# Kernel optimization log

Hardware: AMD Instinct MI355X
Metric: run time of the kernel (lower is better)

Reference implementation:

```python
import jax, jax.numpy as jnp
import numpy as np

N_NODES = 100000
N_EDGES = 262144
IN_DIM = 768
HIDDEN = 256


def setup_inputs() -> dict:
    key = jax.random.key(0)
    ks = jax.random.split(key, 8)
    x_src = jax.random.normal(ks[0], (N_NODES, IN_DIM), dtype=jnp.float32)
    x_dst = jax.random.normal(ks[1], (N_NODES, IN_DIM), dtype=jnp.float32)
    s_idx = jax.random.randint(ks[2], (N_EDGES,), 0, N_NODES, dtype=jnp.int32)
    d_idx = jax.random.randint(ks[3], (N_EDGES,), 0, N_NODES, dtype=jnp.int32)
    # MLP params: Linear(2*in_dim -> hidden), Linear(hidden -> 1)
    lim1 = 1.0 / np.sqrt(2 * IN_DIM)
    W1 = jax.random.uniform(ks[4], (2 * IN_DIM, HIDDEN), minval=-lim1, maxval=lim1, dtype=jnp.float32)
    b1 = jax.random.uniform(ks[5], (HIDDEN,), minval=-lim1, maxval=lim1, dtype=jnp.float32)
    lim2 = 1.0 / np.sqrt(HIDDEN)
    W2 = jax.random.uniform(ks[6], (HIDDEN, 1), minval=-lim2, maxval=lim2, dtype=jnp.float32)
    b2 = jax.random.uniform(ks[7], (1,), minval=-lim2, maxval=lim2, dtype=jnp.float32)
    return {"x_src": x_src, "x_dst": x_dst, "s_idx": s_idx, "d_idx": d_idx,
            "W1": W1, "b1": b1, "W2": W2, "b2": b2}


def reference(x_src, x_dst, s_idx, d_idx, W1, b1, W2, b2):
    # h = concat([x_src[s], x_dst[d]], axis=1) @ W1 + b1
    # Expressed without materializing the [E, 2*in_dim] concat by splitting W1.
    h = (jnp.take(x_src, s_idx, axis=0) @ W1[:IN_DIM]
         + jnp.take(x_dst, d_idx, axis=0) @ W1[IN_DIM:]
         + b1)  # [E, hidden]
    h = jax.nn.relu(h)  # dropout is identity in eval mode
    logits = h @ W2 + b2  # [E, 1]
    return logits.reshape(-1)
```

## Files before the change

### kernel.cpp

```cpp
#include <hip/hip_runtime.h>
#include <hip/hip_bf16.h>

#define N_NODES 100000
#define N_EDGES 262144
#define IN_DIM 768
#define HIDDEN 256
#define BM 256
#define BN 256
#define BK 64
#define NK (IN_DIM / BK)
#define M_BLOCKS 391
#define M_PAD (M_BLOCKS * BM)
#define WT_TILE_BYTES (BN * BK * 2)

typedef __attribute__((ext_vector_type(8))) short short8;
typedef __attribute__((ext_vector_type(4))) float f32x4;

__device__ __forceinline__ unsigned short f32_to_bf16(float f) {
    unsigned int u = __builtin_bit_cast(unsigned int, f);
    u = (u + 0x7FFFu + ((u >> 16) & 1u)) >> 16;
    return (unsigned short)u;
}
__device__ __forceinline__ float bf16_to_f32(unsigned short h) {
    unsigned int u = ((unsigned int)h) << 16;
    return __builtin_bit_cast(float, u);
}
__device__ __forceinline__ void gload_lds16(const void* gsrc, void* lds) {
    __builtin_amdgcn_global_load_lds(
        (const __attribute__((address_space(1))) unsigned int*)gsrc,
        (__attribute__((address_space(3))) unsigned int*)lds,
        16, 0, 0);
}

__global__ __launch_bounds__(256) void convert_w1(const float* __restrict__ W1,
                                                  unsigned short* __restrict__ WtT) {
    int t = blockIdx.x * blockDim.x + threadIdx.x;
    if (t >= 2 * NK * BN * BK) return;
    int g  = t / (NK * BN * BK);
    int r  = t % (NK * BN * BK);
    int ks = r / (BN * BK);
    int r2 = r % (BN * BK);
    int n  = r2 / BK;
    int w  = r2 % BK;
    int c  = w >> 3;
    int j  = w & 7;
    int k  = ks * BK + ((c ^ (n & 7)) << 3) + j;
    WtT[t] = f32_to_bf16(W1[(size_t)(g * IN_DIM + k) * HIDDEN + n]);
}

__global__ __launch_bounds__(512, 2) void node_gemm(const float* __restrict__ X0,
                                                    const float* __restrict__ X1,
                                                    const unsigned short* __restrict__ WtT,
                                                    unsigned short* __restrict__ Pout,
                                                    unsigned short* __restrict__ Qout) {
    const int g = blockIdx.y;
    const float* __restrict__ X = g ? X1 : X0;
    unsigned short* __restrict__ Out = g ? Qout : Pout;
    const char* wt_base = (const char*)WtT + (size_t)g * NK * WT_TILE_BYTES;

    __shared__ unsigned short As[2][BM * BK];
    __shared__ unsigned short Bs[2][BN * BK];

    const int m0   = blockIdx.x * BM;
    const int tid  = threadIdx.x;
    const int lane = tid & 63;
    const int wid  = tid >> 6;
    const int wm   = wid >> 2;
    const int wn   = wid & 3;

    const int ar = tid >> 4;
    const int ap = tid & 15;

    float4 areg[8];
    f32x4 acc[8][4] = {};

    auto load_a = [&](int ks) {
        const int k0 = ks * BK;
#pragma unroll
        for (int p = 0; p < 8; ++p) {
            int r = ar + p * 32;
            int rg = m0 + r;
            if (rg >= N_NODES) rg = N_NODES - 1;
            areg[p] = *(const float4*)(X + (size_t)rg * IN_DIM + k0 + ap * 4);
        }
    };
    auto write_a = [&](int buf) {
        char* base = (char*)As[buf];
#pragma unroll
        for (int p = 0; p < 8; ++p) {
            int r = ar + p * 32;
            float4 v = areg[p];
            ushort4 w;
            w.x = f32_to_bf16(v.x); w.y = f32_to_bf16(v.y);
            w.z = f32_to_bf16(v.z); w.w = f32_to_bf16(v.w);
            *(ushort4*)(base + r * 128 + ((ap * 8) ^ ((r & 7) << 4))) = w;
        }
    };
    auto load_b = [&](int ks, int buf) {
        const char* gsrc = wt_base + (size_t)ks * WT_TILE_BYTES + wid * 4096 + lane * 16;
        char* lbase = (char*)Bs[buf] + wid * 4096;
#pragma unroll
        for (int j = 0; j < 4; ++j)
            gload_lds16(gsrc + j * 1024, lbase + j * 1024);
    };
    auto compute = [&](int buf) {
        const char* a_base = (const char*)As[buf];
        const char* b_base = (const char*)Bs[buf];
#pragma unroll
        for (int kk = 0; kk < 2; ++kk) {
            const int kb = kk * 64 + ((lane >> 4) << 4);
            short8 bfr[4];
#pragma unroll
            for (int ni = 0; ni < 4; ++ni) {
                int n = wn * 64 + ni * 16 + (lane & 15);
                bfr[ni] = *(const short8*)(b_base + n * 128 + (kb ^ ((n & 7) << 4)));
            }
            __builtin_amdgcn_s_setprio(1);
#pragma unroll
            for (int mi = 0; mi < 8; ++mi) {
                int r = wm * 128 + mi * 16 + (lane & 15);
                short8 a = *(const short8*)(a_base + r * 128 + (kb ^ ((r & 7) << 4)));
#pragma unroll
                for (int ni = 0; ni < 4; ++ni)
                    acc[mi][ni] = __builtin_amdgcn_mfma_f32_16x16x32_bf16(
                        bfr[ni], a, acc[mi][ni], 0, 0, 0);
            }
            __builtin_amdgcn_s_setprio(0);
        }
    };

    load_b(0, 0);
    load_a(0);
    write_a(0);
    __syncthreads();
    int cur = 0;
    for (int ks = 0; ks < NK; ++ks) {
        if (ks + 1 < NK) {
            load_b(ks + 1, cur ^ 1);
            load_a(ks + 1);
        }
        compute(cur);
        if (ks + 1 < NK) write_a(cur ^ 1);
        __syncthreads();
        cur ^= 1;
    }

    const int mrow = wm * 128 + (lane & 15);
    const int nb0  = wn * 64 + ((lane >> 4) << 2);
#pragma unroll
    for (int mi = 0; mi < 8; ++mi) {
        size_t mg = (size_t)(m0 + mrow + mi * 16);
#pragma unroll
        for (int ni = 0; ni < 4; ++ni) {
            f32x4 a = acc[mi][ni];
            ushort4 w;
            w.x = f32_to_bf16(a[0]); w.y = f32_to_bf16(a[1]);
            w.z = f32_to_bf16(a[2]); w.w = f32_to_bf16(a[3]);
            *(ushort4*)(Out + mg * HIDDEN + nb0 + ni * 16) = w;
        }
    }
}

__global__ __launch_bounds__(256) void edge_mlp(const unsigned short* __restrict__ P,
                                                const unsigned short* __restrict__ Q,
                                                const int* __restrict__ s_idx,
                                                const int* __restrict__ d_idx,
                                                const float* __restrict__ b1,
                                                const float* __restrict__ W2,
                                                const float* __restrict__ b2,
                                                float* __restrict__ out) {
    const int lane = threadIdx.x & 63;
    const int gw = (blockIdx.x * blockDim.x + threadIdx.x) >> 6;
    const int nw = (gridDim.x * blockDim.x) >> 6;
    const float4 b1v = *(const float4*)(b1 + lane * 4);
    const float4 w2v = *(const float4*)(W2 + lane * 4);
    const float b2s = *b2;
    for (int e = gw; e < N_EDGES; e += nw) {
        int s = s_idx[e];
        int d = d_idx[e];
        ushort4 pv = *(const ushort4*)(P + (size_t)s * HIDDEN + lane * 4);
        ushort4 qv = *(const ushort4*)(Q + (size_t)d * HIDDEN + lane * 4);
        float h, sum;
        h = bf16_to_f32(pv.x) + bf16_to_f32(qv.x) + b1v.x; h = fmaxf(h, 0.f); sum  = h * w2v.x;
        h = bf16_to_f32(pv.y) + bf16_to_f32(qv.y) + b1v.y; h = fmaxf(h, 0.f); sum += h * w2v.y;
        h = bf16_to_f32(pv.z) + bf16_to_f32(qv.z) + b1v.z; h = fmaxf(h, 0.f); sum += h * w2v.z;
        h = bf16_to_f32(pv.w) + bf16_to_f32(qv.w) + b1v.w; h = fmaxf(h, 0.f); sum += h * w2v.w;
#pragma unroll
        for (int off = 32; off; off >>= 1) sum += __shfl_xor(sum, off, 64);
        if (lane == 0) out[e] = sum + b2s;
    }
}

extern "C" void kernel_launch(void* const* d_in, const int* in_sizes, int n_in,
                              void* d_out, int out_size, void* d_ws, size_t ws_size,
                              hipStream_t stream) {
    const float* x_src = (const float*)d_in[0];
    const float* x_dst = (const float*)d_in[1];
    const int*   s_idx = (const int*)d_in[2];
    const int*   d_idx = (const int*)d_in[3];
    const float* W1    = (const float*)d_in[4];
    const float* b1    = (const float*)d_in[5];
    const float* W2    = (const float*)d_in[6];
    const float* b2    = (const float*)d_in[7];
    float* out = (float*)d_out;

    char* ws = (char*)d_ws;
    unsigned short* WtT = (unsigned short*)ws;
    unsigned short* P   = (unsigned short*)(ws + 786432);
    unsigned short* Q   = (unsigned short*)(ws + 786432 + (size_t)M_PAD * HIDDEN * 2);

    convert_w1<<<(2 * NK * BN * BK + 255) / 256, 256, 0, stream>>>(W1, WtT);

    dim3 gg(M_BLOCKS, 2);
    node_gemm<<<gg, 512, 0, stream>>>(x_src, x_dst, WtT, P, Q);

    edge_mlp<<<2048, 256, 0, stream>>>(P, Q, s_idx, d_idx, b1, W2, b2, out);
}
```

Before: 267.8 us.

## Stream fp32 A tiles directly to LDS and convert to bf16 at fragment load

The node GEMM now loads the fp32 X tile straight into LDS with global_load_lds instead of staging it through registers, converting to bf16 while building MFMA fragments. Tiles shrink to BM=128 and BK=32 with a new XOR swizzle for both A and the pre-transposed W1 layout, and the loop becomes a two-stage prefetch pipeline using explicit vmcnt waits and raw barriers. The 4x4 accumulator footprint is meant to allow higher occupancy (launch bound 4). In exchange, the bf16 conversion is redone per wave inside the compute loop, B is reloaded twice as often per output row, and the hand-written waitcnt/barrier scheme is fragile.

```diff
diff --git a/kernel.cpp b/kernel.cpp
--- a/kernel.cpp
+++ b/kernel.cpp
@@ -5,16 +5,19 @@
 #define N_EDGES 262144
 #define IN_DIM 768
 #define HIDDEN 256
-#define BM 256
+#define BM 128
 #define BN 256
-#define BK 64
+#define BK 32
 #define NK (IN_DIM / BK)
-#define M_BLOCKS 391
+#define M_BLOCKS 782
 #define M_PAD (M_BLOCKS * BM)
 #define WT_TILE_BYTES (BN * BK * 2)
 
 typedef __attribute__((ext_vector_type(8))) short short8;
 typedef __attribute__((ext_vector_type(4))) float f32x4;
+
+#define WAITV(n) asm volatile("s_waitcnt vmcnt(" #n ")" ::: "memory")
+#define FENCE()  asm volatile("" ::: "memory")
 
 __device__ __forceinline__ unsigned short f32_to_bf16(float f) {
     unsigned int u = __builtin_bit_cast(unsigned int, f);
@@ -40,15 +43,15 @@
     int r  = t % (NK * BN * BK);
     int ks = r / (BN * BK);
     int r2 = r % (BN * BK);
-    int n  = r2 / BK;
-    int w  = r2 % BK;
-    int c  = w >> 3;
-    int j  = w & 7;
-    int k  = ks * BK + ((c ^ (n & 7)) << 3) + j;
+    int s  = r2 >> 3;
+    int j  = r2 & 7;
+    int n  = s >> 2;
+    int p  = s & 3;
+    int k  = ks * BK + ((p ^ ((n >> 1) & 3)) << 3) + j;
     WtT[t] = f32_to_bf16(W1[(size_t)(g * IN_DIM + k) * HIDDEN + n]);
 }
 
-__global__ __launch_bounds__(512, 2) void node_gemm(const float* __restrict__ X0,
+__global__ __launch_bounds__(512, 4) void node_gemm(const float* __restrict__ X0,
                                                     const float* __restrict__ X1,
                                                     const unsigned short* __restrict__ WtT,
                                                     unsigned short* __restrict__ Pout,
@@ -58,8 +61,8 @@
     unsigned short* __restrict__ Out = g ? Qout : Pout;
     const char* wt_base = (const char*)WtT + (size_t)g * NK * WT_TILE_BYTES;
 
-    __shared__ unsigned short As[2][BM * BK];
-    __shared__ unsigned short Bs[2][BN * BK];
+    __shared__ __attribute__((aligned(16))) char As[2][BM * BK * 4];
+    __shared__ __attribute__((aligned(16))) char Bs[2][BN * BK * 2];
 
     const int m0   = blockIdx.x * BM;
     const int tid  = threadIdx.x;
@@ -68,87 +71,84 @@
     const int wm   = wid >> 2;
     const int wn   = wid & 3;
 
-    const int ar = tid >> 4;
-    const int ap = tid & 15;
-
-    float4 areg[8];
-    f32x4 acc[8][4] = {};
-
-    auto load_a = [&](int ks) {
+    f32x4 acc[4][4] = {};
+
+    const int a_row_in_inst = lane >> 3;
+    const int a_perm        = ((lane & 7) ^ a_row_in_inst) << 2;
+
+    auto issue = [&](int ks, int buf) {
         const int k0 = ks * BK;
 #pragma unroll
-        for (int p = 0; p < 8; ++p) {
-            int r = ar + p * 32;
+        for (int j = 0; j < 2; ++j) {
+            int r  = (wid * 2 + j) * 8 + a_row_in_inst;
             int rg = m0 + r;
             if (rg >= N_NODES) rg = N_NODES - 1;
-            areg[p] = *(const float4*)(X + (size_t)rg * IN_DIM + k0 + ap * 4);
-        }
+            gload_lds16(X + (size_t)rg * IN_DIM + k0 + a_perm,
+                        As[buf] + (wid * 2 + j) * 1024);
+        }
+        const char* src = wt_base + (size_t)ks * WT_TILE_BYTES + (wid * 2) * 1024 + lane * 16;
+#pragma unroll
+        for (int j = 0; j < 2; ++j)
+            gload_lds16(src + j * 1024, Bs[buf] + (wid * 2 + j) * 1024);
     };
-    auto write_a = [&](int buf) {
-        char* base = (char*)As[buf];
-#pragma unroll
-        for (int p = 0; p < 8; ++p) {
-            int r = ar + p * 32;
-            float4 v = areg[p];
-            ushort4 w;
-            w.x = f32_to_bf16(v.x); w.y = f32_to_bf16(v.y);
-            w.z = f32_to_bf16(v.z); w.w = f32_to_bf16(v.w);
-            *(ushort4*)(base + r * 128 + ((ap * 8) ^ ((r & 7) << 4))) = w;
-        }
+
+    auto compute = [&](int buf) {
+        const char* ab = As[buf];
+        const char* bb = Bs[buf];
+        const int lr = lane & 15;
+        const int c  = lane >> 4;
+        short8 bfr[4];
+#pragma unroll
+        for (int ni = 0; ni < 4; ++ni) {
+            int n = wn * 64 + ni * 16 + lr;
+            bfr[ni] = *(const short8*)(bb + n * 64 + ((c ^ ((n >> 1) & 3)) << 4));
+        }
+        __builtin_amdgcn_s_setprio(1);
+#pragma unroll
+        for (int mi = 0; mi < 4; ++mi) {
+            int r = wm * 64 + mi * 16 + lr;
+            const char* rowp = ab + r * 128;
+            float4 lo = *(const float4*)(rowp + (((2 * c)     ^ (r & 7)) << 4));
+            float4 hi = *(const float4*)(rowp + (((2 * c + 1) ^ (r & 7)) << 4));
+            short8 a;
+            a[0] = f32_to_bf16(lo.x); a[1] = f32_to_bf16(lo.y);
+            a[2] = f32_to_bf16(lo.z); a[3] = f32_to_bf16(lo.w);
+            a[4] = f32_to_bf16(hi.x); a[5] = f32_to_bf16(hi.y);
+            a[6] = f32_to_bf16(hi.z); a[7] = f32_to_bf16(hi.w);
+#pragma unroll
+            for (int ni = 0; ni < 4; ++ni)
+                acc[mi][ni] = __builtin_amdgcn_mfma_f32_16x16x32_bf16(
+                    bfr[ni], a, acc[mi][ni], 0, 0, 0);
+        }
+        __builtin_amdgcn_s_setprio(0);
     };
-    auto load_b = [&](int ks, int buf) {
-        const char* gsrc = wt_base + (size_t)ks * WT_TILE_BYTES + wid * 4096 + lane * 16;
-        char* lbase = (char*)Bs[buf] + wid * 4096;
-#pragma unroll
-        for (int j = 0; j < 4; ++j)
-            gload_lds16(gsrc + j * 1024, lbase + j * 1024);
-    };
-    auto compute = [&](int buf) {
-        const char* a_base = (const char*)As[buf];
-        const char* b_base = (const char*)Bs[buf];
-#pragma unroll
-        for (int kk = 0; kk < 2; ++kk) {
-            const int kb = kk * 64 + ((lane >> 4) << 4);
-            short8 bfr[4];
-#pragma unroll
-            for (int ni = 0; ni < 4; ++ni) {
-                int n = wn * 64 + ni * 16 + (lane & 15);
-                bfr[ni] = *(const short8*)(b_base + n * 128 + (kb ^ ((n & 7) << 4)));
-            }
-            __builtin_amdgcn_s_setprio(1);
-#pragma unroll
-            for (int mi = 0; mi < 8; ++mi) {
-                int r = wm * 128 + mi * 16 + (lane & 15);
-                short8 a = *(const short8*)(a_base + r * 128 + (kb ^ ((r & 7) << 4)));
-#pragma unroll
-                for (int ni = 0; ni < 4; ++ni)
-                    acc[mi][ni] = __builtin_amdgcn_mfma_f32_16x16x32_bf16(
-                        bfr[ni], a, acc[mi][ni], 0, 0, 0);
-            }
-            __builtin_amdgcn_s_setprio(0);
-        }
-    };
-
-    load_b(0, 0);
-    load_a(0);
-    write_a(0);
-    __syncthreads();
-    int cur = 0;
+
+    issue(0, 0);
+    issue(1, 1);
+    WAITV(4);
+    __builtin_amdgcn_s_barrier();
+    FENCE();
+
     for (int ks = 0; ks < NK; ++ks) {
-        if (ks + 1 < NK) {
-            load_b(ks + 1, cur ^ 1);
-            load_a(ks + 1);
-        }
-        compute(cur);
-        if (ks + 1 < NK) write_a(cur ^ 1);
-        __syncthreads();
-        cur ^= 1;
+        const int buf = ks & 1;
+        compute(buf);
+        FENCE();
+        __builtin_amdgcn_s_barrier();
+        FENCE();
+        if (ks + 2 < NK) {
+            issue(ks + 2, buf);
+            WAITV(4);
+        } else {
+            WAITV(0);
+        }
+        __builtin_amdgcn_s_barrier();
+        FENCE();
     }
 
-    const int mrow = wm * 128 + (lane & 15);
+    const int mrow = wm * 64 + (lane & 15);
     const int nb0  = wn * 64 + ((lane >> 4) << 2);
 #pragma unroll
-    for (int mi = 0; mi < 8; ++mi) {
+    for (int mi = 0; mi < 4; ++mi) {
         size_t mg = (size_t)(m0 + mrow + mi * 16);
 #pragma unroll
         for (int ni = 0; ni < 4; ++ni) {
```

After: 251.5 us. 1.06x faster.

## Restructure node GEMM main loop into fine-grained interleaved load/MFMA schedule

Applied to the files above, without the earlier changes.

Rewrites the node_gemm K-loop into a manually scheduled pipeline. A tiles are prefetched two tiles ahead through registers in halves, and each tile is split into four MFMA phases. Global loads, LDS writes and barriers are interleaved between those phases, with explicit vmcnt/lgkmcnt waits. A loads now use 32-byte contiguous chunks per thread, and the B-weight conversion index math is simplified. The aim is to hide HBM latency of the fp32 X stream behind matrix work. The cost is more barriers per tile and fragile hand-tuned waitcnt ordering.

```diff
diff --git a/kernel.cpp b/kernel.cpp
--- a/kernel.cpp
+++ b/kernel.cpp
@@ -16,6 +16,10 @@
 typedef __attribute__((ext_vector_type(8))) short short8;
 typedef __attribute__((ext_vector_type(4))) float f32x4;
 
+#define WAITV(n) asm volatile("s_waitcnt vmcnt(" #n ")" ::: "memory")
+#define LGKM0()  asm volatile("s_waitcnt lgkmcnt(0)" ::: "memory")
+#define BAR()    __builtin_amdgcn_s_barrier()
+
 __device__ __forceinline__ unsigned short f32_to_bf16(float f) {
     unsigned int u = __builtin_bit_cast(unsigned int, f);
     u = (u + 0x7FFFu + ((u >> 16) & 1u)) >> 16;
@@ -37,14 +41,12 @@
     int t = blockIdx.x * blockDim.x + threadIdx.x;
     if (t >= 2 * NK * BN * BK) return;
     int g  = t / (NK * BN * BK);
-    int r  = t % (NK * BN * BK);
-    int ks = r / (BN * BK);
-    int r2 = r % (BN * BK);
-    int n  = r2 / BK;
-    int w  = r2 % BK;
-    int c  = w >> 3;
-    int j  = w & 7;
-    int k  = ks * BK + ((c ^ (n & 7)) << 3) + j;
+    int r  = t - g * (NK * BN * BK);
+    int kt = r >> 14;
+    int n  = (r >> 6) & 255;
+    int p  = (r >> 3) & 7;
+    int j  = r & 7;
+    int k  = kt * BK + ((p ^ (n & 7)) << 3) + j;
     WtT[t] = f32_to_bf16(W1[(size_t)(g * IN_DIM + k) * HIDDEN + n]);
 }
 
@@ -58,8 +60,8 @@
     unsigned short* __restrict__ Out = g ? Qout : Pout;
     const char* wt_base = (const char*)WtT + (size_t)g * NK * WT_TILE_BYTES;
 
-    __shared__ unsigned short As[2][BM * BK];
-    __shared__ unsigned short Bs[2][BN * BK];
+    __shared__ __attribute__((aligned(16))) char As[2][BM * BK * 2];
+    __shared__ __attribute__((aligned(16))) char Bs[2][BN * BK * 2];
 
     const int m0   = blockIdx.x * BM;
     const int tid  = threadIdx.x;
@@ -67,86 +69,115 @@
     const int wid  = tid >> 6;
     const int wm   = wid >> 2;
     const int wn   = wid & 3;
-
-    const int ar = tid >> 4;
-    const int ap = tid & 15;
-
-    float4 areg[8];
+    const int lr   = lane & 15;
+    const int c    = lane >> 4;
+
+    const int srow = wid * 32 + (lane >> 3);
+    const int g8   = lane & 7;
+
     f32x4 acc[8][4] = {};
-
-    auto load_a = [&](int ks) {
-        const int k0 = ks * BK;
-#pragma unroll
-        for (int p = 0; p < 8; ++p) {
-            int r = ar + p * 32;
+    float4 st[4][2];
+
+    auto loadA_half = [&](int kt, int h) {
+        const int k0 = kt * BK;
+#pragma unroll
+        for (int q = 2 * h; q < 2 * h + 2; ++q) {
+            int r  = srow + q * 8;
             int rg = m0 + r;
             if (rg >= N_NODES) rg = N_NODES - 1;
-            areg[p] = *(const float4*)(X + (size_t)rg * IN_DIM + k0 + ap * 4);
-        }
-    };
-    auto write_a = [&](int buf) {
-        char* base = (char*)As[buf];
-#pragma unroll
-        for (int p = 0; p < 8; ++p) {
-            int r = ar + p * 32;
-            float4 v = areg[p];
-            ushort4 w;
-            w.x = f32_to_bf16(v.x); w.y = f32_to_bf16(v.y);
-            w.z = f32_to_bf16(v.z); w.w = f32_to_bf16(v.w);
-            *(ushort4*)(base + r * 128 + ((ap * 8) ^ ((r & 7) << 4))) = w;
-        }
-    };
-    auto load_b = [&](int ks, int buf) {
-        const char* gsrc = wt_base + (size_t)ks * WT_TILE_BYTES + wid * 4096 + lane * 16;
-        char* lbase = (char*)Bs[buf] + wid * 4096;
+            const float* p = X + (size_t)rg * IN_DIM + k0 + g8 * 8;
+            st[q][0] = *(const float4*)(p);
+            st[q][1] = *(const float4*)(p + 4);
+        }
+    };
+    auto writeA = [&](char* wrA) {
+#pragma unroll
+        for (int q = 0; q < 4; ++q) {
+            int r  = srow + q * 8;
+            int gs = g8 ^ (r & 7);
+            short8 w;
+            w[0] = (short)f32_to_bf16(st[q][0].x); w[1] = (short)f32_to_bf16(st[q][0].y);
+            w[2] = (short)f32_to_bf16(st[q][0].z); w[3] = (short)f32_to_bf16(st[q][0].w);
+            w[4] = (short)f32_to_bf16(st[q][1].x); w[5] = (short)f32_to_bf16(st[q][1].y);
+            w[6] = (short)f32_to_bf16(st[q][1].z); w[7] = (short)f32_to_bf16(st[q][1].w);
+            *(short8*)(wrA + r * 128 + (gs << 4)) = w;
+        }
+    };
+    auto issueB = [&](int kt, char* wrB) {
+        const char* src = wt_base + (size_t)kt * WT_TILE_BYTES + wid * 4096 + lane * 16;
+        char* dst = wrB + wid * 4096;
 #pragma unroll
         for (int j = 0; j < 4; ++j)
-            gload_lds16(gsrc + j * 1024, lbase + j * 1024);
-    };
-    auto compute = [&](int buf) {
-        const char* a_base = (const char*)As[buf];
-        const char* b_base = (const char*)Bs[buf];
-#pragma unroll
-        for (int kk = 0; kk < 2; ++kk) {
-            const int kb = kk * 64 + ((lane >> 4) << 4);
-            short8 bfr[4];
-#pragma unroll
-            for (int ni = 0; ni < 4; ++ni) {
-                int n = wn * 64 + ni * 16 + (lane & 15);
-                bfr[ni] = *(const short8*)(b_base + n * 128 + (kb ^ ((n & 7) << 4)));
-            }
-            __builtin_amdgcn_s_setprio(1);
-#pragma unroll
-            for (int mi = 0; mi < 8; ++mi) {
-                int r = wm * 128 + mi * 16 + (lane & 15);
-                short8 a = *(const short8*)(a_base + r * 128 + (kb ^ ((r & 7) << 4)));
-#pragma unroll
-                for (int ni = 0; ni < 4; ++ni)
-                    acc[mi][ni] = __builtin_amdgcn_mfma_f32_16x16x32_bf16(
-                        bfr[ni], a, acc[mi][ni], 0, 0, 0);
-            }
-            __builtin_amdgcn_s_setprio(0);
-        }
-    };
-
-    load_b(0, 0);
-    load_a(0);
-    write_a(0);
-    __syncthreads();
-    int cur = 0;
-    for (int ks = 0; ks < NK; ++ks) {
-        if (ks + 1 < NK) {
-            load_b(ks + 1, cur ^ 1);
-            load_a(ks + 1);
-        }
-        compute(cur);
-        if (ks + 1 < NK) write_a(cur ^ 1);
-        __syncthreads();
-        cur ^= 1;
+            gload_lds16(src + j * 1024, dst + j * 1024);
+    };
+    auto readA = [&](const char* rdA, int kk, short8 (&afr)[8]) {
+#pragma unroll
+        for (int mi = 0; mi < 8; ++mi) {
+            int r  = wm * 128 + mi * 16 + lr;
+            int gs = (kk * 4 + c) ^ (r & 7);
+            afr[mi] = *(const short8*)(rdA + r * 128 + (gs << 4));
+        }
+    };
+    auto readB = [&](const char* rdB, int ni, int kk) -> short8 {
+        int n  = wn * 64 + ni * 16 + lr;
+        int gs = (kk * 4 + c) ^ (n & 7);
+        return *(const short8*)(rdB + n * 128 + (gs << 4));
+    };
+    auto mfma16 = [&](const short8 (&afr)[8], const short8 b0, const short8 b1, int nb) {
+        __builtin_amdgcn_s_setprio(1);
+#pragma unroll
+        for (int mi = 0; mi < 8; ++mi) {
+            acc[mi][nb]     = __builtin_amdgcn_mfma_f32_16x16x32_bf16(b0, afr[mi], acc[mi][nb], 0, 0, 0);
+            acc[mi][nb + 1] = __builtin_amdgcn_mfma_f32_16x16x32_bf16(b1, afr[mi], acc[mi][nb + 1], 0, 0, 0);
+        }
+        __builtin_amdgcn_s_setprio(0);
+    };
+
+    auto tile = [&](int t, const char* rdA, const char* rdB, char* wrA, char* wrB) {
+        const int kB = (t + 1 < NK) ? t + 1 : NK - 1;
+        const int kA = (t + 2 < NK) ? t + 2 : NK - 1;
+        short8 afr[8], b0, b1;
+        readA(rdA, 0, afr);
+        b0 = readB(rdB, 0, 0); b1 = readB(rdB, 1, 0);
+        issueB(kB, wrB);
+        BAR(); LGKM0();
+        mfma16(afr, b0, b1, 0);
+        BAR();
+        b0 = readB(rdB, 2, 0); b1 = readB(rdB, 3, 0);
+        WAITV(4);
+        writeA(wrA);
+        BAR(); LGKM0();
+        mfma16(afr, b0, b1, 2);
+        BAR();
+        readA(rdA, 1, afr);
+        b0 = readB(rdB, 0, 1); b1 = readB(rdB, 1, 1);
+        loadA_half(kA, 0);
+        BAR(); LGKM0();
+        mfma16(afr, b0, b1, 0);
+        BAR();
+        b0 = readB(rdB, 2, 1); b1 = readB(rdB, 3, 1);
+        loadA_half(kA, 1);
+        WAITV(8);
+        BAR(); LGKM0();
+        mfma16(afr, b0, b1, 2);
+        BAR();
+    };
+
+    loadA_half(0, 0); loadA_half(0, 1);
+    issueB(0, Bs[0]);
+    WAITV(0);
+    writeA(As[0]);
+    loadA_half(1, 0); loadA_half(1, 1);
+    LGKM0();
+    BAR();
+
+    for (int t2 = 0; t2 < NK; t2 += 2) {
+        tile(t2,     As[0], Bs[0], As[1], Bs[1]);
+        tile(t2 + 1, As[1], Bs[1], As[0], Bs[0]);
     }
 
-    const int mrow = wm * 128 + (lane & 15);
-    const int nb0  = wn * 64 + ((lane >> 4) << 2);
+    const int mrow = wm * 128 + lr;
+    const int nb0  = wn * 64 + (c << 2);
 #pragma unroll
     for (int mi = 0; mi < 8; ++mi) {
         size_t mg = (size_t)(m0 + mrow + mi * 16);
@@ -159,6 +190,7 @@
             *(ushort4*)(Out + mg * HIDDEN + nb0 + ni * 16) = w;
         }
     }
+    WAITV(0);
 }
 
 __global__ __launch_bounds__(256) void edge_mlp(const unsigned short* __restrict__ P,
```

Result: no change. 272.7 us (+1.8%).
